# Kernel tuning notes

Hardware: AMD Instinct MI355X
Metric: run time of the kernel (lower is better)

Reference implementation:

```python
import jax, jax.numpy as jnp
import numpy as np

EPS = 1e-5
KC = 256  # key_channels


def conv1x1(x, w):
    # x: [N,Cin,H,W], w: [Cout,Cin] -> [N,Cout,H,W]
    return jnp.einsum('nchw,oc->nohw', x, w)


def bn_relu(x, g, b, m, v):
    # eval-mode BatchNorm2d + ReLU, fused affine form
    inv = g / jnp.sqrt(v + EPS)
    return jax.nn.relu(x * inv[None, :, None, None] + (b - m * inv)[None, :, None, None])


def setup_inputs() -> dict:
    key = jax.random.key(0)
    ks = jax.random.split(key, 8)
    N, C, H, W, K = 8, 512, 128, 128, 19
    d = {
        'x': jax.random.normal(ks[0], (N, C, H, W), jnp.float32),
        'proxy': jax.random.normal(ks[1], (N, C, K, 1), jnp.float32),
        'w_p1': jax.random.normal(ks[2], (KC, C), jnp.float32) / np.sqrt(C),
        'w_p2': jax.random.normal(ks[3], (KC, KC), jnp.float32) / np.sqrt(KC),
        'w_o1': jax.random.normal(ks[4], (KC, C), jnp.float32) / np.sqrt(C),
        'w_o2': jax.random.normal(ks[5], (KC, KC), jnp.float32) / np.sqrt(KC),
        'w_d': jax.random.normal(ks[6], (KC, C), jnp.float32) / np.sqrt(C),
        'w_u': jax.random.normal(ks[7], (C, KC), jnp.float32) / np.sqrt(KC),
    }
    for pfx, ch in [('p1', KC), ('p2', KC), ('o1', KC), ('o2', KC), ('d', KC), ('u', C)]:
        d[f'{pfx}_g'] = jnp.ones((ch,), jnp.float32)
        d[f'{pfx}_b'] = jnp.zeros((ch,), jnp.float32)
        d[f'{pfx}_m'] = jnp.zeros((ch,), jnp.float32)
        d[f'{pfx}_v'] = jnp.ones((ch,), jnp.float32)
    return d


def reference(x, proxy, w_p1, p1_g, p1_b, p1_m, p1_v, w_p2, p2_g, p2_b, p2_m, p2_v,
              w_o1, o1_g, o1_b, o1_m, o1_v, w_o2, o2_g, o2_b, o2_m, o2_v,
              w_d, d_g, d_b, d_m, d_v, w_u, u_g, u_b, u_m, u_v):
    N, C, H, W = x.shape
    # f_pixel: conv1x1 -> BN+ReLU -> conv1x1 -> BN+ReLU
    q = bn_relu(conv1x1(bn_relu(conv1x1(x, w_p1), p1_g, p1_b, p1_m, p1_v), w_p2),
                p2_g, p2_b, p2_m, p2_v)                       # [N,KC,H,W]
    k = bn_relu(conv1x1(bn_relu(conv1x1(proxy, w_o1), o1_g, o1_b, o1_m, o1_v), w_o2),
                o2_g, o2_b, o2_m, o2_v)                       # [N,KC,K,1]
    v = bn_relu(conv1x1(proxy, w_d), d_g, d_b, d_m, d_v)      # [N,KC,K,1]

    query = q.reshape(N, KC, H * W).transpose(0, 2, 1)        # [N,HW,KC]
    keym = k.reshape(N, KC, -1)                               # [N,KC,K]
    value = v.reshape(N, KC, -1).transpose(0, 2, 1)           # [N,K,KC]

    sim = jnp.einsum('nlc,nck->nlk', query, keym) * (KC ** -0.5)  # [N,HW,K]
    sim = jax.nn.softmax(sim, axis=-1)
    context = jnp.einsum('nlk,nkc->nlc', sim, value)          # [N,HW,KC]
    context = context.transpose(0, 2, 1).reshape(N, KC, H, W)
    # f_up
    return bn_relu(conv1x1(context, w_u), u_g, u_b, u_m, u_v)  # [N,C,H,W]
```

## Files before the change

kernel.cpp:

```cpp
#include <hip/hip_runtime.h>

#define HW     16384
#define CIN    512
#define KCH    256
#define NKEY   19
#define NKP    32
#define NBATCH 8

typedef __attribute__((ext_vector_type(8))) short s16x8;
typedef __attribute__((ext_vector_type(4))) short s16x4;
typedef __attribute__((ext_vector_type(4))) float f32x4;

__device__ __forceinline__ short f2bf(float f) {
  union { float f; unsigned u; } x;
  x.f = f;
  unsigned r = x.u + 0x7fffu + ((x.u >> 16) & 1u);
  return (short)(r >> 16);
}

#define BARRIER_ND() do { \
    __builtin_amdgcn_sched_barrier(0); \
    asm volatile("s_waitcnt lgkmcnt(0)" ::: "memory"); \
    __builtin_amdgcn_s_barrier(); \
    __builtin_amdgcn_sched_barrier(0); \
  } while (0)

__global__ __launch_bounds__(256) void kprepA(
    const float* __restrict__ proxy,
    const float* __restrict__ w_p1, const float* __restrict__ w_p2,
    const float* __restrict__ p1g, const float* __restrict__ p1b,
    const float* __restrict__ p1m, const float* __restrict__ p1v,
    const float* __restrict__ p2g, const float* __restrict__ p2b,
    const float* __restrict__ p2m, const float* __restrict__ p2v,
    const float* __restrict__ ug,  const float* __restrict__ ub,
    const float* __restrict__ um,  const float* __restrict__ uvv,
    const float* __restrict__ w_o1, const float* __restrict__ w_d,
    const float* __restrict__ o1g, const float* __restrict__ o1b,
    const float* __restrict__ o1m, const float* __restrict__ o1v,
    const float* __restrict__ dg,  const float* __restrict__ db,
    const float* __restrict__ dm,  const float* __restrict__ dv,
    short* __restrict__ W1L, short* __restrict__ W2L,
    float* __restrict__ b1, float* __restrict__ b2, float* __restrict__ bu,
    float* __restrict__ t_o1g, float* __restrict__ vmatg)
{
  __shared__ char PB[32 * 1024];
  const int tid = threadIdx.x;
  if (blockIdx.x < 772) {
    int t = blockIdx.x * 256 + tid;
    if (t < 131072) {
      int kf = t >> 13, rem = t & 8191, tt = rem >> 9, e512 = rem & 511;
      int l = e512 >> 3, e = e512 & 7;
      int m = tt * 16 + (l & 15);
      int kcol = kf * 32 + (l >> 4) * 8 + e;
      float inv = p1g[m] * rsqrtf(p1v[m] + 1e-5f);
      W1L[t] = f2bf(inv * w_p1[(size_t)m * CIN + kcol]);
    } else if (t < 196608) {
      int u = t - 131072;
      int kf = u >> 13, rem = u & 8191, tt = rem >> 9, e512 = rem & 511;
      int l = e512 >> 3, e = e512 & 7;
      int m = tt * 16 + (l & 15);
      int kcol = kf * 32 + (l >> 4) * 8 + e;
      float inv = p2g[m] * rsqrtf(p2v[m] + 1e-5f);
      W2L[u] = f2bf(inv * w_p2[(size_t)m * KCH + kcol]);
    } else if (t < 196608 + 256) {
      int o = t - 196608;
      float inv = p1g[o] * rsqrtf(p1v[o] + 1e-5f);
      b1[o] = p1b[o] - p1m[o] * inv;
    } else if (t < 196608 + 512) {
      int o = t - 196608 - 256;
      float inv = p2g[o] * rsqrtf(p2v[o] + 1e-5f);
      b2[o] = p2b[o] - p2m[o] * inv;
    } else if (t < 196608 + 1024) {
      int o = t - 196608 - 512;
      float inv = ug[o] * rsqrtf(uvv[o] + 1e-5f);
      bu[o] = ub[o] - um[o] * inv;
    }
    return;
  }
  int bid = blockIdx.x - 772;
  int sel = bid >> 5;
  int r5  = bid & 31;
  int n   = r5 >> 2;
  int mbase = (r5 & 3) << 6;

  for (int j = 0; j < 8; ++j) *(s16x8*)(PB + (tid + j * 256) * 16) = (s16x8)0;
  __syncthreads();
  const float* pn = proxy + (size_t)n * CIN * NKEY;
  for (int e = tid; e < CIN * NKEY; e += 256) {
    int c = e / NKEY, k = e - c * NKEY;
    *(short*)(PB + k * 1024 + ((c << 1) ^ ((k & 7) << 4))) = f2bf(pn[e]);
  }
  __syncthreads();

  const int w = tid >> 6, lane = tid & 63, g = lane >> 4, i = lane & 15;
  const float* W  = sel ? w_d : w_o1;
  const float* gg = sel ? dg : o1g;
  const float* bb = sel ? db : o1b;
  const float* mm = sel ? dm : o1m;
  const float* vv = sel ? dv : o1v;
  f32x4 acc2[2];
  acc2[0] = (f32x4)0.f; acc2[1] = (f32x4)0.f;
  const int arow = mbase + w * 16 + i;
#pragma unroll 1
  for (int kf = 0; kf < 16; ++kf) {
    const float* wp = W + (size_t)arow * CIN + kf * 32 + g * 8;
    f32x4 a0 = *(const f32x4*)wp, a1 = *(const f32x4*)(wp + 4);
    s16x8 af;
#pragma unroll
    for (int e = 0; e < 4; ++e) { af[e] = f2bf(a0[e]); af[e + 4] = f2bf(a1[e]); }
#pragma unroll
    for (int nj = 0; nj < 2; ++nj) {
      int key = nj * 16 + i;
      s16x8 bf = *(const s16x8*)(PB + key * 1024 + ((kf * 64 + g * 16) ^ ((key & 7) << 4)));
      acc2[nj] = __builtin_amdgcn_mfma_f32_16x16x32_bf16(af, bf, acc2[nj], 0, 0, 0);
    }
  }
  float* dst = (sel ? vmatg : t_o1g) + (size_t)n * 8192;
#pragma unroll
  for (int r = 0; r < 4; ++r) {
    int o = mbase + w * 16 + g * 4 + r;
    float inv = gg[o] * rsqrtf(vv[o] + 1e-5f);
    float beta = bb[o] - mm[o] * inv;
#pragma unroll
    for (int nj = 0; nj < 2; ++nj) {
      int key = nj * 16 + i;
      dst[key * 256 + o] = fmaxf(acc2[nj][r] * inv + beta, 0.f);
    }
  }
}

__global__ __launch_bounds__(256) void kprepB(
    const float* __restrict__ w_o2, const float* __restrict__ w_u,
    const float* __restrict__ o2g, const float* __restrict__ o2b,
    const float* __restrict__ o2m, const float* __restrict__ o2v,
    const float* __restrict__ ug,  const float* __restrict__ uvv,
    const float* __restrict__ t_o1g, const float* __restrict__ vmatg,
    short* __restrict__ KmL, short* __restrict__ WuL)
{
  __shared__ char TB[32 * 512];
  const int tid = threadIdx.x;
  const int isKm = (blockIdx.x < 32);
  int n, mbase;
  const float* src;
  if (isKm) { n = blockIdx.x >> 2; mbase = (blockIdx.x & 3) << 6; src = t_o1g; }
  else { int b2_ = blockIdx.x - 32; n = b2_ >> 3; mbase = (b2_ & 7) << 6; src = vmatg; }
  const float* sn = src + (size_t)n * 8192;
  for (int j = 0; j < 32; ++j) {
    int idx = tid + j * 256;
    int key = idx >> 8, o = idx & 255;
    *(short*)(TB + key * 512 + ((o << 1) ^ ((key & 7) << 4))) = f2bf(sn[idx]);
  }
  __syncthreads();

  const int w = tid >> 6, lane = tid & 63, g = lane >> 4, i = lane & 15;
  const float* W = isKm ? w_o2 : w_u;
  f32x4 acc2[2];
  acc2[0] = (f32x4)0.f; acc2[1] = (f32x4)0.f;
  const int arow = mbase + w * 16 + i;
#pragma unroll 1
  for (int kf = 0; kf < 8; ++kf) {
    const float* wp = W + (size_t)arow * KCH + kf * 32 + g * 8;
    f32x4 a0 = *(const f32x4*)wp, a1 = *(const f32x4*)(wp + 4);
    s16x8 af;
#pragma unroll
    for (int e = 0; e < 4; ++e) { af[e] = f2bf(a0[e]); af[e + 4] = f2bf(a1[e]); }
#pragma unroll
    for (int nj = 0; nj < 2; ++nj) {
      int key = nj * 16 + i;
      s16x8 bf = *(const s16x8*)(TB + key * 512 + ((kf * 64 + g * 16) ^ ((key & 7) << 4)));
      acc2[nj] = __builtin_amdgcn_mfma_f32_16x16x32_bf16(af, bf, acc2[nj], 0, 0, 0);
    }
  }
  if (isKm) {
    short* Kn = KmL + (size_t)n * 8192;
#pragma unroll
    for (int r = 0; r < 4; ++r) {
      int o2 = mbase + w * 16 + g * 4 + r;
      float inv = o2g[o2] * rsqrtf(o2v[o2] + 1e-5f);
      float beta = o2b[o2] - o2m[o2] * inv;
#pragma unroll
      for (int nj = 0; nj < 2; ++nj) {
        float val = fmaxf(acc2[nj][r] * inv + beta, 0.f) * 0.0625f;
        Kn[((o2 >> 5) * 2 + nj) * 512 + (((o2 >> 3) & 3) * 16 + i) * 8 + (o2 & 7)] = f2bf(val);
      }
    }
  } else {
    short* Wn = WuL + (size_t)n * 16384;
#pragma unroll
    for (int r = 0; r < 4; ++r) {
      int c = mbase + w * 16 + g * 4 + r;
      float inv = ug[c] * rsqrtf(uvv[c] + 1e-5f);
#pragma unroll
      for (int nj = 0; nj < 2; ++nj) {
        int key = nj * 16 + i;
        float val = acc2[nj][r] * inv;
        Wn[(c >> 4) * 512 + ((key >> 3) * 16 + (c & 15)) * 8 + (key & 7)] = f2bf(val);
      }
    }
  }
}

#define LOADCHUNK(R, ck) do { \
    const float* xp = xb + (size_t)((ck) * 64 + scb) * HW; \
    _Pragma("unroll") \
    for (int ii = 0; ii < 16; ++ii) (R)[ii] = xp[(size_t)ii * HW]; \
  } while (0)

#define WRITECHUNK(R, ck) do { \
    s16x8 h0, h1; \
    _Pragma("unroll") \
    for (int ii = 0; ii < 8; ++ii) { h0[ii] = f2bf((R)[ii]); h1[ii] = f2bf((R)[ii + 8]); } \
    char* wr_ = smem + ((ck) % 3) * 8192 + sp * 128; \
    *(s16x8*)(wr_ + (((scb << 1) +  0) ^ ssw)) = h0; \
    *(s16x8*)(wr_ + (((scb << 1) + 16) ^ ssw)) = h1; \
  } while (0)

#define MFMASTEP(ck) do { \
    const char* rb_ = smem + ((ck) % 3) * 8192; \
    _Pragma("unroll") \
    for (int ks = 0; ks < 2; ++ks) { \
      s16x8 af[4], bf[4]; \
      _Pragma("unroll") \
      for (int mi = 0; mi < 4; ++mi) \
        af[mi] = *(const s16x8*)(W1L + ((((ck) * 2 + ks) * 16 + (w * 4 + mi)) << 9) + (lane << 3)); \
      _Pragma("unroll") \
      for (int ni = 0; ni < 4; ++ni) { \
        int p_ = ni * 16 + i; \
        bf[ni] = *(const s16x8*)(rb_ + p_ * 128 + (((ks * 32 + g * 8) << 1) ^ ((p_ & 7) << 4))); \
      } \
      _Pragma("unroll") \
      for (int mi = 0; mi < 4; ++mi) \
        _Pragma("unroll") \
        for (int ni = 0; ni < 4; ++ni) \
          acc[mi][ni] = __builtin_amdgcn_mfma_f32_16x16x32_bf16(af[mi], bf[ni], acc[mi][ni], 0, 0, 0); \
    } \
  } while (0)

__global__ __launch_bounds__(256, 4) void k_main(
    const float* __restrict__ x,
    const short* __restrict__ W1L, const short* __restrict__ W2L,
    const short* __restrict__ KmL, const short* __restrict__ WuL,
    const float* __restrict__ b1, const float* __restrict__ b2,
    const float* __restrict__ bu,
    float* __restrict__ out)
{
  __shared__ char smem[32768];
  char* t1q = smem;

  const int tid  = threadIdx.x;
  const int w    = tid >> 6;
  const int lane = tid & 63;
  const int g    = lane >> 4;
  const int i    = lane & 15;
  const int n    = blockIdx.x >> 8;
  const int l0   = (blockIdx.x & 255) << 6;

  f32x4 acc[4][4];
#pragma unroll
  for (int a_ = 0; a_ < 4; ++a_)
#pragma unroll
    for (int b_ = 0; b_ < 4; ++b_) acc[a_][b_] = (f32x4)0.f;

  const int sp  = lane;
  const int scb = w << 4;
  const int ssw = (sp & 7) << 4;
  const float* xb = x + (size_t)n * CIN * HW + l0 + sp;

  float RA[16], RB[16];
  LOADCHUNK(RA, 0);
  LOADCHUNK(RB, 1);
  WRITECHUNK(RA, 0);
  BARRIER_ND();

#pragma unroll
  for (int cp = 0; cp < 4; ++cp) {
    const int cka = 2 * cp, ckb = 2 * cp + 1;
    if (cka + 2 < 8) LOADCHUNK(RA, cka + 2);
    MFMASTEP(cka);
    WRITECHUNK(RB, ckb);
    BARRIER_ND();
    if (ckb + 2 < 8) LOADCHUNK(RB, ckb + 2);
    MFMASTEP(ckb);
    if (ckb + 1 < 8) WRITECHUNK(RA, ckb + 1);
    BARRIER_ND();
  }

#pragma unroll
  for (int mi = 0; mi < 4; ++mi) {
    f32x4 bias = *(const f32x4*)(b1 + w * 64 + mi * 16 + g * 4);
#pragma unroll
    for (int ni = 0; ni < 4; ++ni) {
      int p = ni * 16 + i;
      s16x4 hh;
#pragma unroll
      for (int r = 0; r < 4; ++r) hh[r] = f2bf(fmaxf(acc[mi][ni][r] + bias[r], 0.f));
      *(s16x4*)(t1q + p * 512 + (((w * 64 + mi * 16 + g * 4) << 1) ^ ((p & 7) << 4))) = hh;
      acc[mi][ni] = (f32x4)0.f;
    }
  }
  __syncthreads();

#pragma unroll 1
  for (int ks = 0; ks < 8; ++ks) {
    s16x8 af[4], bf[4];
#pragma unroll
    for (int mi = 0; mi < 4; ++mi)
      af[mi] = *(const s16x8*)(W2L + (((ks * 16) + (w * 4 + mi)) << 9) + (lane << 3));
#pragma unroll
    for (int ni = 0; ni < 4; ++ni) {
      int p = ni * 16 + i;
      bf[ni] = *(const s16x8*)(t1q + p * 512 + (((ks * 32 + g * 8) << 1) ^ ((p & 7) << 4)));
    }
#pragma unroll
    for (int mi = 0; mi < 4; ++mi)
#pragma unroll
      for (int ni = 0; ni < 4; ++ni)
        acc[mi][ni] = __builtin_amdgcn_mfma_f32_16x16x32_bf16(af[mi], bf[ni], acc[mi][ni], 0, 0, 0);
  }
  __syncthreads();
#pragma unroll
  for (int mi = 0; mi < 4; ++mi) {
    f32x4 bias = *(const f32x4*)(b2 + w * 64 + mi * 16 + g * 4);
#pragma unroll
    for (int ni = 0; ni < 4; ++ni) {
      int p = ni * 16 + i;
      s16x4 hh;
#pragma unroll
      for (int r = 0; r < 4; ++r) hh[r] = f2bf(fmaxf(acc[mi][ni][r] + bias[r], 0.f));
      *(s16x4*)(t1q + p * 512 + (((w * 64 + mi * 16 + g * 4) << 1) ^ ((p & 7) << 4))) = hh;
    }
  }
  __syncthreads();

  f32x4 as_[2];
  as_[0] = (f32x4)0.f; as_[1] = (f32x4)0.f;
  const short* Kn = KmL + (size_t)n * 8192;
  const int ps = (w << 4) | i;
  const int psw = (ps & 7) << 4;
#pragma unroll
  for (int ks = 0; ks < 8; ++ks) {
    s16x8 bq = *(const s16x8*)(t1q + ps * 512 + (((ks * 32 + g * 8) << 1) ^ psw));
#pragma unroll
    for (int mi = 0; mi < 2; ++mi) {
      s16x8 ak = *(const s16x8*)(Kn + (((ks * 2 + mi)) << 9) + (lane << 3));
      as_[mi] = __builtin_amdgcn_mfma_f32_16x16x32_bf16(ak, bq, as_[mi], 0, 0, 0);
    }
  }
  float mx = -1e30f;
#pragma unroll
  for (int mi = 0; mi < 2; ++mi)
#pragma unroll
    for (int r = 0; r < 4; ++r) {
      int k = mi * 16 + g * 4 + r;
      if (k < NKEY) mx = fmaxf(mx, as_[mi][r]);
    }
  mx = fmaxf(mx, __shfl_xor(mx, 16, 64));
  mx = fmaxf(mx, __shfl_xor(mx, 32, 64));
  float e[2][4];
  float sum = 0.f;
#pragma unroll
  for (int mi = 0; mi < 2; ++mi)
#pragma unroll
    for (int r = 0; r < 4; ++r) {
      int k = mi * 16 + g * 4 + r;
      float t = (k < NKEY) ? __expf(as_[mi][r] - mx) : 0.f;
      e[mi][r] = t;
      sum += t;
    }
  sum += __shfl_xor(sum, 16, 64);
  sum += __shfl_xor(sum, 32, 64);
  float rs = 1.f / sum;
  __syncthreads();
  char* P = smem;
#pragma unroll
  for (int mi = 0; mi < 2; ++mi) {
    s16x4 hh;
#pragma unroll
    for (int r = 0; r < 4; ++r) hh[r] = f2bf(e[mi][r] * rs);
    *(s16x4*)(P + ps * 64 + (((mi * 16 + g * 4) << 1) ^ ((ps & 3) << 4))) = hh;
  }
  __syncthreads();

  s16x8 bP[4];
#pragma unroll
  for (int ni = 0; ni < 4; ++ni) {
    int p = ni * 16 + i;
    bP[ni] = *(const s16x8*)(P + p * 64 + ((g * 16) ^ ((p & 3) << 4)));
  }
  const short* Wn = WuL + (size_t)n * 16384;
  float* op = out + (size_t)n * CIN * HW + l0;
#pragma unroll
  for (int mi = 0; mi < 8; ++mi) {
    int row0 = w * 128 + mi * 16;
    s16x8 aU = *(const s16x8*)(Wn + ((w * 8 + mi) << 9) + (lane << 3));
    f32x4 bias = *(const f32x4*)(bu + row0 + g * 4);
#pragma unroll
    for (int ni = 0; ni < 4; ++ni) {
      f32x4 o4 = __builtin_amdgcn_mfma_f32_16x16x32_bf16(aU, bP[ni], bias, 0, 0, 0);
#pragma unroll
      for (int r = 0; r < 4; ++r)
        op[(size_t)(row0 + g * 4 + r) * HW + ni * 16 + i] = fmaxf(o4[r], 0.f);
    }
  }
}

extern "C" void kernel_launch(void* const* d_in, const int* in_sizes, int n_in,
                              void* d_out, int out_size, void* d_ws, size_t ws_size,
                              hipStream_t stream) {
  (void)in_sizes; (void)n_in; (void)out_size; (void)ws_size;
  const float* x     = (const float*)d_in[0];
  const float* proxy = (const float*)d_in[1];
  const float* w_p1  = (const float*)d_in[2];
  const float* w_p2  = (const float*)d_in[3];
  const float* w_o1  = (const float*)d_in[4];
  const float* w_o2  = (const float*)d_in[5];
  const float* w_d   = (const float*)d_in[6];
  const float* w_u   = (const float*)d_in[7];
  const float* p1g = (const float*)d_in[8],  *p1b = (const float*)d_in[9];
  const float* p1m = (const float*)d_in[10], *p1v = (const float*)d_in[11];
  const float* p2g = (const float*)d_in[12], *p2b = (const float*)d_in[13];
  const float* p2m = (const float*)d_in[14], *p2v = (const float*)d_in[15];
  const float* o1g = (const float*)d_in[16], *o1b = (const float*)d_in[17];
  const float* o1m = (const float*)d_in[18], *o1v = (const float*)d_in[19];
  const float* o2g = (const float*)d_in[20], *o2b = (const float*)d_in[21];
  const float* o2m = (const float*)d_in[22], *o2v = (const float*)d_in[23];
  const float* dg  = (const float*)d_in[24], *db  = (const float*)d_in[25];
  const float* dm  = (const float*)d_in[26], *dv  = (const float*)d_in[27];
  const float* ug  = (const float*)d_in[28], *ub  = (const float*)d_in[29];
  const float* um  = (const float*)d_in[30], *uv  = (const float*)d_in[31];

  char* ws = (char*)d_ws;
  short* W1L    = (short*)(ws + 0);
  short* W2L    = (short*)(ws + 262144);
  short* KmL    = (short*)(ws + 393216);
  short* WuL    = (short*)(ws + 524288);
  float* b1     = (float*)(ws + 786432);
  float* b2     = (float*)(ws + 787456);
  float* bu     = (float*)(ws + 788480);
  float* t_o1g  = (float*)(ws + 790528);
  float* vmatg  = (float*)(ws + 1052672);

  kprepA<<<836, 256, 0, stream>>>(proxy,
                                  w_p1, w_p2, p1g, p1b, p1m, p1v,
                                  p2g, p2b, p2m, p2v, ug, ub, um, uv,
                                  w_o1, w_d, o1g, o1b, o1m, o1v,
                                  dg, db, dm, dv,
                                  W1L, W2L, b1, b2, bu, t_o1g, vmatg);
  kprepB<<<96, 256, 0, stream>>>(w_o2, w_u, o2g, o2b, o2m, o2v, ug, uv,
                                 t_o1g, vmatg, KmL, WuL);
  k_main<<<2048, 256, 0, stream>>>(x, W1L, W2L, KmL, WuL, b1, b2, bu, (float*)d_out);
}
```

Measured before the change: 197.5 us.

## Restructure first GEMM staging to larger double-buffered K chunks

```diff
diff --git a/kernel.cpp b/kernel.cpp
--- a/kernel.cpp
+++ b/kernel.cpp
@@ -17,13 +17,6 @@
   unsigned r = x.u + 0x7fffu + ((x.u >> 16) & 1u);
   return (short)(r >> 16);
 }
-
-#define BARRIER_ND() do { \
-    __builtin_amdgcn_sched_barrier(0); \
-    asm volatile("s_waitcnt lgkmcnt(0)" ::: "memory"); \
-    __builtin_amdgcn_s_barrier(); \
-    __builtin_amdgcn_sched_barrier(0); \
-  } while (0)
 
 __global__ __launch_bounds__(256) void kprepA(
     const float* __restrict__ proxy,
@@ -201,32 +194,34 @@
 }
 
 #define LOADCHUNK(R, ck) do { \
-    const float* xp = xb + (size_t)((ck) * 64 + scb) * HW; \
+    const float* xp = xb + (size_t)((ck) * 128 + scb) * HW; \
     _Pragma("unroll") \
-    for (int ii = 0; ii < 16; ++ii) (R)[ii] = xp[(size_t)ii * HW]; \
+    for (int ii = 0; ii < 32; ++ii) (R)[ii] = xp[(size_t)ii * HW]; \
   } while (0)
 
 #define WRITECHUNK(R, ck) do { \
-    s16x8 h0, h1; \
+    char* wr_ = smem + (((ck) & 1) << 14) + sp * 256; \
     _Pragma("unroll") \
-    for (int ii = 0; ii < 8; ++ii) { h0[ii] = f2bf((R)[ii]); h1[ii] = f2bf((R)[ii + 8]); } \
-    char* wr_ = smem + ((ck) % 3) * 8192 + sp * 128; \
-    *(s16x8*)(wr_ + (((scb << 1) +  0) ^ ssw)) = h0; \
-    *(s16x8*)(wr_ + (((scb << 1) + 16) ^ ssw)) = h1; \
+    for (int j = 0; j < 4; ++j) { \
+      s16x8 h; \
+      _Pragma("unroll") \
+      for (int e = 0; e < 8; ++e) h[e] = f2bf((R)[j * 8 + e]); \
+      *(s16x8*)(wr_ + ((scb2 + j * 16) ^ ssw)) = h; \
+    } \
   } while (0)
 
 #define MFMASTEP(ck) do { \
-    const char* rb_ = smem + ((ck) % 3) * 8192; \
+    const char* rb_ = smem + (((ck) & 1) << 14); \
     _Pragma("unroll") \
-    for (int ks = 0; ks < 2; ++ks) { \
+    for (int ks = 0; ks < 4; ++ks) { \
       s16x8 af[4], bf[4]; \
       _Pragma("unroll") \
       for (int mi = 0; mi < 4; ++mi) \
-        af[mi] = *(const s16x8*)(W1L + ((((ck) * 2 + ks) * 16 + (w * 4 + mi)) << 9) + (lane << 3)); \
+        af[mi] = *(const s16x8*)(W1L + ((((ck) * 4 + ks) * 16 + (w * 4 + mi)) << 9) + (lane << 3)); \
       _Pragma("unroll") \
       for (int ni = 0; ni < 4; ++ni) { \
         int p_ = ni * 16 + i; \
-        bf[ni] = *(const s16x8*)(rb_ + p_ * 128 + (((ks * 32 + g * 8) << 1) ^ ((p_ & 7) << 4))); \
+        bf[ni] = *(const s16x8*)(rb_ + p_ * 256 + ((ks * 64 + g * 16) ^ ((p_ & 7) << 4))); \
       } \
       _Pragma("unroll") \
       for (int mi = 0; mi < 4; ++mi) \
@@ -261,28 +256,23 @@
 #pragma unroll
     for (int b_ = 0; b_ < 4; ++b_) acc[a_][b_] = (f32x4)0.f;
 
-  const int sp  = lane;
-  const int scb = w << 4;
-  const int ssw = (sp & 7) << 4;
+  const int sp   = lane;
+  const int scb  = w << 5;
+  const int scb2 = w << 6;
+  const int ssw  = (sp & 7) << 4;
   const float* xb = x + (size_t)n * CIN * HW + l0 + sp;
 
-  float RA[16], RB[16];
+  float RA[32];
   LOADCHUNK(RA, 0);
-  LOADCHUNK(RB, 1);
   WRITECHUNK(RA, 0);
-  BARRIER_ND();
-
-#pragma unroll
-  for (int cp = 0; cp < 4; ++cp) {
-    const int cka = 2 * cp, ckb = 2 * cp + 1;
-    if (cka + 2 < 8) LOADCHUNK(RA, cka + 2);
-    MFMASTEP(cka);
-    WRITECHUNK(RB, ckb);
-    BARRIER_ND();
-    if (ckb + 2 < 8) LOADCHUNK(RB, ckb + 2);
-    MFMASTEP(ckb);
-    if (ckb + 1 < 8) WRITECHUNK(RA, ckb + 1);
-    BARRIER_ND();
+  __syncthreads();
+
+#pragma unroll
+  for (int ck = 0; ck < 4; ++ck) {
+    if (ck < 3) LOADCHUNK(RA, ck + 1);
+    MFMASTEP(ck);
+    if (ck < 3) WRITECHUNK(RA, ck + 1);
+    __syncthreads();
   }
 
 #pragma unroll
```

Result: no change. 197.1 us (-0.2%).
